# Kernel tuning notes

Hardware: AMD Instinct MI355X
Metric: run time of the kernel (lower is better)

The kernel has to match this reference:

```python
import jax, jax.numpy as jnp
import numpy as np

N, E, G = 50000, 1600000, 512
IN, HID, PROJ = 128, 128, 256


def setup_inputs() -> dict:
    key = jax.random.key(0)
    ks = jax.random.split(key, 20)
    s = 0.05
    return {
        'x1': jax.random.normal(ks[0], (N, IN), jnp.float32),
        'edge_index1': jax.random.randint(ks[1], (2, E), 0, N),
        'batch1': jnp.sort(jax.random.randint(ks[2], (N,), 0, G)),
        'x2': jax.random.normal(ks[3], (N, IN), jnp.float32),
        'edge_index2': jax.random.randint(ks[4], (2, E), 0, N),
        'batch2': jnp.sort(jax.random.randint(ks[5], (N,), 0, G)),
        'W1': jax.random.normal(ks[6], (IN, HID), jnp.float32) * s,
        'b1': jnp.zeros((HID,), jnp.float32),
        'W2': jax.random.normal(ks[7], (HID, HID), jnp.float32) * s,
        'b2': jnp.zeros((HID,), jnp.float32),
        'W3': jax.random.normal(ks[8], (HID, HID), jnp.float32) * s,
        'b3': jnp.zeros((HID,), jnp.float32),
        'Wp1': jax.random.normal(ks[9], (HID, PROJ), jnp.float32) * s,
        'bp1': jnp.zeros((PROJ,), jnp.float32),
        'gamma1': jnp.ones((PROJ,), jnp.float32),
        'beta1': jnp.zeros((PROJ,), jnp.float32),
        'Wp2': jax.random.normal(ks[10], (PROJ, PROJ), jnp.float32) * s,
        'bp2': jnp.zeros((PROJ,), jnp.float32),
        'gamma2': jnp.ones((PROJ,), jnp.float32),
        'beta2': jnp.zeros((PROJ,), jnp.float32),
        'Wq1': jax.random.normal(ks[11], (PROJ, PROJ // 2), jnp.float32) * s,
        'bq1': jnp.zeros((PROJ // 2,), jnp.float32),
        'Wq2': jax.random.normal(ks[12], (PROJ // 2, PROJ), jnp.float32) * s,
        'bq2': jnp.zeros((PROJ,), jnp.float32),
    }


def _gcn_conv(x, src, dst, W, b):
    # PyG GCNConv: add self-loops, symmetric norm, gather -> scatter-add
    n = x.shape[0]
    h = x @ W                                   # [n, out]
    loop = jnp.arange(n)
    s = jnp.concatenate([src, loop])
    d = jnp.concatenate([dst, loop])
    deg = jax.ops.segment_sum(jnp.ones(s.shape[0], h.dtype), d, num_segments=n)
    dinv = jnp.where(deg > 0, 1.0 / jnp.sqrt(deg), 0.0)
    norm = (dinv[s] * dinv[d])[:, None]         # [E+n, 1]
    out = jax.ops.segment_sum(h[s] * norm, d, num_segments=n)
    return out + b


def _encode(x, edge_index, batch, W1, b1, W2, b2, W3, b3):
    src, dst = edge_index[0], edge_index[1]
    h = jax.nn.relu(_gcn_conv(x, src, dst, W1, b1))
    h = jax.nn.relu(_gcn_conv(h, src, dst, W2, b2)) + h
    h = jax.nn.relu(_gcn_conv(h, src, dst, W3, b3)) + h
    # global mean pool over graph ids
    s = jax.ops.segment_sum(h, batch, num_segments=G)
    cnt = jax.ops.segment_sum(jnp.ones(h.shape[0], h.dtype), batch, num_segments=G)
    return s / jnp.maximum(cnt, 1.0)[:, None]


def _batchnorm(x, gamma, beta):
    m = x.mean(axis=0)
    v = x.var(axis=0)  # biased, matches torch BN normalization
    return gamma * (x - m) / jnp.sqrt(v + 1e-5) + beta


def _projector(h, Wp1, bp1, g1, be1, Wp2, bp2, g2, be2):
    z = jax.nn.relu(_batchnorm(h @ Wp1 + bp1, g1, be1))
    return _batchnorm(z @ Wp2 + bp2, g2, be2)


def _predictor(z, Wq1, bq1, Wq2, bq2):
    return jax.nn.relu(z @ Wq1 + bq1) @ Wq2 + bq2


def reference(x1, edge_index1, batch1, x2, edge_index2, batch2,
              W1, b1, W2, b2, W3, b3,
              Wp1, bp1, gamma1, beta1, Wp2, bp2, gamma2, beta2,
              Wq1, bq1, Wq2, bq2):
    h1 = _encode(x1, edge_index1, batch1, W1, b1, W2, b2, W3, b3)
    h2 = _encode(x2, edge_index2, batch2, W1, b1, W2, b2, W3, b3)
    z1 = _projector(h1, Wp1, bp1, gamma1, beta1, Wp2, bp2, gamma2, beta2)
    z2 = _projector(h2, Wp1, bp1, gamma1, beta1, Wp2, bp2, gamma2, beta2)
    p1 = _predictor(z1, Wq1, bq1, Wq2, bq2)
    p2 = _predictor(z2, Wq1, bq1, Wq2, bq2)
    return (p1, p2, z1, z2)
```

## Files before the change

kernel.cpp:

```cpp
#include <hip/hip_runtime.h>
#include <hip/hip_bf16.h>

#define NN     50000
#define NN2    100000
#define NEDGE  1600000
#define NE2    3200000
#define NG     512
#define FIN    128
#define FHID   128
#define FPROJ  256

#define BSH    9
#define BSZ    512
#define NBUCK  98
#define NBUCK2 196
#define EPB    8192
#define NABLK  196
#define NABLK2 392
#define NHIST2 (NBUCK2*NABLK2)
#define NSB1   ((NHIST2 + 255) / 256)

#define SRCSH  12
#define NKEY   (BSZ * 16)

#define MAXE_BLK 2048

typedef __attribute__((ext_vector_type(8))) short short8;
typedef __attribute__((ext_vector_type(4))) float f32x4;
typedef __attribute__((ext_vector_type(2))) float f32x2;

static __device__ __forceinline__ short f2bf(float f) {
    union { float f; unsigned u; } x; x.f = f;
    unsigned r = (x.u + 0x7FFFu + ((x.u >> 16) & 1u)) >> 16;
    return (short)(r & 0xFFFFu);
}
static __device__ __forceinline__ float bf2f(unsigned short u) {
    union { unsigned u; float f; } x; x.u = ((unsigned)u) << 16;
    return x.f;
}
static __device__ __forceinline__ float bflo(unsigned u) {
    union { unsigned u; float f; } x; x.u = u << 16; return x.f;
}
static __device__ __forceinline__ float bfhi(unsigned u) {
    union { unsigned u; float f; } x; x.u = u & 0xFFFF0000u; return x.f;
}
static __device__ __forceinline__ unsigned packbf(float a, float b) {
    return (unsigned)(unsigned short)f2bf(a) | ((unsigned)(unsigned short)f2bf(b) << 16);
}
static __device__ __forceinline__ f32x2 bfpair(unsigned u) {
    union { unsigned v[2]; f32x2 f; } x;
    x.v[0] = u << 16;
    x.v[1] = u & 0xFFFF0000u;
    return x.f;
}


__global__ __launch_bounds__(1024) void k_bhist(const int* __restrict__ dst0,
                                                const int* __restrict__ dst1,
                                                int* __restrict__ histG,
                                                unsigned short* __restrict__ lrank,
                                                const float* __restrict__ W0,
                                                const float* __restrict__ W1,
                                                const float* __restrict__ W2,
                                                short* __restrict__ Wf) {
    if (blockIdx.x >= NABLK2) {
        int w = (blockIdx.x - NABLK2) * 1024 + threadIdx.x;
        int l = w >> 11;
        int t = w & 2047;
        int b = t >> 6;
        int lane = t & 63;
        const float* W = (l == 0) ? W0 : (l == 1) ? W1 : W2;
        int nt = b >> 2, kt = b & 3;
        int n = nt * 16 + (lane & 15);
        int kbase = kt * 32 + (lane >> 4) * 8;
        short8 v;
#pragma unroll
        for (int j = 0; j < 8; ++j) v[j] = f2bf(W[(kbase + j) * FHID + n]);
        *(short8*)(Wf + (size_t)l * 16384 + (size_t)((nt * 4 + kt) * 64 + lane) * 8) = v;
        return;
    }
    __shared__ int h[NBUCK2];
    for (int j = threadIdx.x; j < NBUCK2; j += 1024) h[j] = 0;
    __syncthreads();
    int b = blockIdx.x;
    int g = b / NABLK, blk = b % NABLK;
    const int* dst = g ? dst1 : dst0;
    int base = blk * EPB;
    int gb = g * NBUCK;
    for (int t = threadIdx.x; t < EPB; t += 1024) {
        int i = base + t;
        if (i < NEDGE)
            lrank[(size_t)g * NEDGE + i] =
                (unsigned short)atomicAdd(&h[gb + (dst[i] >> BSH)], 1);
    }
    __syncthreads();
    for (int j = threadIdx.x; j < NBUCK2; j += 1024)
        histG[(size_t)j * NABLK2 + b] = h[j];
}

__global__ void s_scan256(const int* __restrict__ in, int* __restrict__ out,
                          int* __restrict__ bsum, int n) {
    __shared__ int s[256];
    int i = blockIdx.x * 256 + threadIdx.x;
    int v = (i < n) ? in[i] : 0;
    s[threadIdx.x] = v;
    for (int o = 1; o < 256; o <<= 1) {
        __syncthreads();
        int t = (threadIdx.x >= o) ? s[threadIdx.x - o] : 0;
        __syncthreads();
        s[threadIdx.x] += t;
    }
    __syncthreads();
    if (i < n) out[i] = s[threadIdx.x] - v;
    if (threadIdx.x == 255) bsum[blockIdx.x] = s[255];
}

__global__ __launch_bounds__(512) void s_scan_tail(int* __restrict__ bsum, int nb) {
    __shared__ int s[512];
    int v = (threadIdx.x < nb) ? bsum[threadIdx.x] : 0;
    s[threadIdx.x] = v;
    for (int o = 1; o < 512; o <<= 1) {
        __syncthreads();
        int t = (threadIdx.x >= o) ? s[threadIdx.x - o] : 0;
        __syncthreads();
        s[threadIdx.x] += t;
    }
    __syncthreads();
    if (threadIdx.x < nb) bsum[threadIdx.x] = s[threadIdx.x] - v;
}

__global__ void s_add(int* __restrict__ out, const int* __restrict__ bs, int n) {
    int i = blockIdx.x * 256 + threadIdx.x;
    if (i < n) out[i] += bs[blockIdx.x];
}

__global__ __launch_bounds__(1024) void k_part(const int* __restrict__ src0,
                                               const int* __restrict__ dst0,
                                               const int* __restrict__ src1,
                                               const int* __restrict__ dst1,
                                               const unsigned short* __restrict__ lrank,
                                               const int* __restrict__ histS,
                                               unsigned* __restrict__ pedge) {
    int b = blockIdx.x;
    int g = b / NABLK, blk = b % NABLK;
    const int* src = g ? src1 : src0;
    const int* dst = g ? dst1 : dst0;
    int base = blk * EPB;
    int gb = g * NBUCK;
    for (int t = threadIdx.x; t < EPB; t += 1024) {
        int i = base + t;
        if (i < NEDGE) {
            int d = dst[i];
            int pos = histS[(size_t)(gb + (d >> BSH)) * NABLK2 + b]
                      + (int)lrank[(size_t)g * NEDGE + i];
            pedge[pos] = (unsigned)src[i] | ((unsigned)(d & (BSZ - 1)) << 16);
        }
    }
}

__global__ __launch_bounds__(512) void k_csr(const unsigned* __restrict__ pedge,
                                             const int* __restrict__ histS,
                                             int* __restrict__ csroff,
                                             unsigned short* __restrict__ csrc,
                                             float* __restrict__ dinv) {
    __shared__ int cnt[NKEY];
    __shared__ int part[512];
    int k = blockIdx.x;
    int g = k / NBUCK;
    int nl0 = (k - g * NBUCK) * BSZ;
    int beg = histS[(size_t)k * NABLK2];
    int end = (k == NBUCK2 - 1) ? NE2 : histS[(size_t)(k + 1) * NABLK2];
    int t = threadIdx.x;
    for (int j = t; j < NKEY; j += 512) cnt[j] = 0;
    __syncthreads();
    for (int e = beg + t; e < end; e += 512) {
        unsigned v = pedge[e];
        int key = (int)((v >> 16) << 4) | (int)((v & 0xFFFFu) >> SRCSH);
        atomicAdd(&cnt[key], 1);
    }
    __syncthreads();
    int base = t * 16;
    int s = 0;
#pragma unroll
    for (int j = 0; j < 16; ++j) s += cnt[base + j];
    part[t] = s;
    for (int o = 1; o < 512; o <<= 1) {
        __syncthreads();
        int v2 = (t >= o) ? part[t - o] : 0;
        __syncthreads();
        part[t] += v2;
    }
    __syncthreads();
    int run = part[t] - s;
#pragma unroll
    for (int j = 0; j < 16; ++j) { int c = cnt[base + j]; cnt[base + j] = run; run += c; }
    __syncthreads();
    {
        int nl = nl0 + t;
        if (nl < NN) {
            int gn = g * NN + nl;
            int d0 = cnt[t * 16];
            int d1 = (t == BSZ - 1) ? (end - beg) : cnt[(t + 1) * 16];
            csroff[gn] = beg + d0;
            dinv[gn] = 1.0f / sqrtf((float)(d1 - d0 + 1));
        }
    }
    __syncthreads();
    for (int e = beg + t; e < end; e += 512) {
        unsigned v = pedge[e];
        int key = (int)((v >> 16) << 4) | (int)((v & 0xFFFFu) >> SRCSH);
        int r = atomicAdd(&cnt[key], 1);
        csrc[beg + r] = (unsigned short)(v & 0xFFFFu);
    }
    if (k == NBUCK2 - 1 && t == 0) csroff[NN2] = NE2;
}


__global__ __launch_bounds__(256) void k_gemm(const float* __restrict__ x1,
                                              const float* __restrict__ x2,
                                              const unsigned short* __restrict__ Abf,
                                              const short* __restrict__ Wf,
                                              const float* __restrict__ dinv,
                                              unsigned short* __restrict__ hp) {
    int lane = threadIdx.x & 63;
    int wv = threadIdx.x >> 6;
    int quad = lane >> 4;
    int rowbase = blockIdx.x * 64 + wv * 16;
    int arow = rowbase + (lane & 15);
    if (arow >= NN2) arow = NN2 - 1;

    f32x4 acc[8];
#pragma unroll
    for (int i = 0; i < 8; ++i) acc[i] = (f32x4){0.f, 0.f, 0.f, 0.f};

#pragma unroll
    for (int kt = 0; kt < 4; ++kt) {
        short8 af;
        if (Abf) {
            af = *(const short8*)(Abf + (size_t)arow * FIN + kt * 32 + quad * 8);
        } else {
            const float* ap = (arow < NN ? x1 + (size_t)arow * FIN
                                         : x2 + (size_t)(arow - NN) * FIN)
                              + kt * 32 + quad * 8;
            float4 a0 = *(const float4*)ap;
            float4 a1 = *(const float4*)(ap + 4);
            af[0] = f2bf(a0.x); af[1] = f2bf(a0.y); af[2] = f2bf(a0.z); af[3] = f2bf(a0.w);
            af[4] = f2bf(a1.x); af[5] = f2bf(a1.y); af[6] = f2bf(a1.z); af[7] = f2bf(a1.w);
        }
#pragma unroll
        for (int nt = 0; nt < 8; ++nt) {
            short8 bf = *(const short8*)(Wf + (size_t)((nt * 4 + kt) * 64 + lane) * 8);
            acc[nt] = __builtin_amdgcn_mfma_f32_16x16x32_bf16(af, bf, acc[nt], 0, 0, 0);
        }
    }
    float4 dv = *(const float4*)(dinv + rowbase + quad * 4);
    float dvv[4] = {dv.x, dv.y, dv.z, dv.w};
    int col = lane & 15;
#pragma unroll
    for (int r = 0; r < 4; ++r) {
        int orow = rowbase + quad * 4 + r;
        if (orow < NN2) {
#pragma unroll
            for (int nt = 0; nt < 8; ++nt)
                hp[(size_t)orow * FHID + nt * 16 + col] =
                    (unsigned short)f2bf(acc[nt][r] * dvv[r]);
        }
    }
}


#define RDI(S, EE) { _Pragma("unroll") for (int j = 0; j < 4; ++j) S[j] = (int)sidx[(EE) + j]; }
#define GTH(V, S)  { _Pragma("unroll") for (int j = 0; j < 4; ++j) V[j] = hpg[(size_t)S[j] * 16 + l16]; }
#define ACC4(V)    { _Pragma("unroll") for (int j = 0; j < 4; ++j) { \
                       a0 += bfpair(V[j].x); a1 += bfpair(V[j].y);   \
                       a2 += bfpair(V[j].z); a3 += bfpair(V[j].w); } }

__global__ __launch_bounds__(256) void k_agg(const uint4* __restrict__ hp4,
                                             const int* __restrict__ off,
                                             const unsigned short* __restrict__ csrc,
                                             const float* __restrict__ dinv,
                                             const float* __restrict__ bias,
                                             const unsigned short* __restrict__ resid,
                                             unsigned short* __restrict__ hout) {
    __shared__ unsigned short sidx[MAXE_BLK + 16];
    int tid = threadIdx.x;
    int l16 = tid & 15;
    int grp = tid >> 4;
    int gnb = blockIdx.x * 16;
    int blkBeg = off[gnb];
    int blkLen = off[gnb + 16] - blkBeg;
    if (blkLen > MAXE_BLK) blkLen = MAXE_BLK;
    for (int i = tid; i < blkLen; i += 256)
        sidx[i] = csrc[blkBeg + i];
    __syncthreads();

    int gn = gnb + grp;
    int g = gn >= NN;
    int node = gn - g * NN;
    const uint4* hpg = hp4 + (size_t)g * NN * 16;
    int beg = off[gn], end = off[gn + 1];
    int lbeg = beg - blkBeg;

    uint4 sv = hpg[(size_t)node * 16 + l16];
    f32x2 a0 = (f32x2){0.f, 0.f}, a1 = (f32x2){0.f, 0.f};
    f32x2 a2 = (f32x2){0.f, 0.f}, a3 = (f32x2){0.f, 0.f};

    int n4 = (end - beg) >> 2;
    if (n4 >= 2) {
        int s0[4], s1[4];
        uint4 v0[4], v1[4];
        int e = lbeg;
        RDI(s0, e);
        RDI(s1, e + 4);
        GTH(v0, s0);
        e += 8;
        int k = 1;
        while (k + 2 <= n4) {
            GTH(v1, s1);
            RDI(s0, e); e += 4;
            ACC4(v0);
            GTH(v0, s0);
            RDI(s1, e); e += 4;
            ACC4(v1);
            k += 2;
        }
        if (k < n4) {
            GTH(v1, s1);
            ACC4(v0);
            ACC4(v1);
        } else {
            ACC4(v0);
        }
    } else if (n4 == 1) {
        int s0[4]; uint4 v0[4];
        RDI(s0, lbeg);
        GTH(v0, s0);
        ACC4(v0);
    }
    int et = lbeg + (n4 << 2), lend = lbeg + (end - beg);
    for (; et < lend; ++et) {
        uint4 w = hpg[(size_t)sidx[et] * 16 + l16];
        a0 += bfpair(w.x); a1 += bfpair(w.y); a2 += bfpair(w.z); a3 += bfpair(w.w);
    }
    a0 += bfpair(sv.x); a1 += bfpair(sv.y); a2 += bfpair(sv.z); a3 += bfpair(sv.w);

    float dv = dinv[gn];
    float4 b0 = ((const float4*)bias)[l16 * 2];
    float4 b1 = ((const float4*)bias)[l16 * 2 + 1];
    float o0 = fmaxf(a0.x * dv + b0.x, 0.f);
    float o1 = fmaxf(a0.y * dv + b0.y, 0.f);
    float o2 = fmaxf(a1.x * dv + b0.z, 0.f);
    float o3 = fmaxf(a1.y * dv + b0.w, 0.f);
    float o4 = fmaxf(a2.x * dv + b1.x, 0.f);
    float o5 = fmaxf(a2.y * dv + b1.y, 0.f);
    float o6 = fmaxf(a3.x * dv + b1.z, 0.f);
    float o7 = fmaxf(a3.y * dv + b1.w, 0.f);
    if (resid) {
        uint4 rv = ((const uint4*)resid)[(size_t)gn * 16 + l16];
        o0 += bflo(rv.x); o1 += bfhi(rv.x);
        o2 += bflo(rv.y); o3 += bfhi(rv.y);
        o4 += bflo(rv.z); o5 += bfhi(rv.z);
        o6 += bflo(rv.w); o7 += bfhi(rv.w);
    }
    uint4 ov;
    ov.x = packbf(o0, o1);
    ov.y = packbf(o2, o3);
    ov.z = packbf(o4, o5);
    ov.w = packbf(o6, o7);
    ((uint4*)hout)[(size_t)gn * 16 + l16] = ov;
}


static __device__ __forceinline__ int lbound(const int* __restrict__ a, int key) {
    int lo = 0, hi = NN;
    while (lo < hi) { int mid = (lo + hi) >> 1; if (a[mid] < key) lo = mid + 1; else hi = mid; }
    return lo;
}

__global__ void k_pool(const unsigned short* __restrict__ h,
                       const int* __restrict__ b0, const int* __restrict__ b1,
                       float* __restrict__ pooled, float* __restrict__ stats) {
    int b = blockIdx.x;
    int g = b >> 9, lg = b & 511;
    int c = threadIdx.x;
    if (b == 0) {
        for (int i = c; i < 2048; i += 128) stats[i] = 0.f;
    }
    const int* batch = g ? b1 : b0;
    int beg = lbound(batch, lg);
    int end = lbound(batch, lg + 1);
    const unsigned short* hb = h + (size_t)g * NN * FHID;
    float s = 0.f;
    for (int i = beg; i < end; ++i) s += bf2f(hb[(size_t)i * FHID + c]);
    int cnt = end - beg;
    pooled[(size_t)b * FHID + c] = s / (float)(cnt > 0 ? cnt : 1);
}


template<int NC>
__global__ __launch_bounds__(256) void k_head(const float* __restrict__ A,
                                              const float* __restrict__ W,
                                              const float* __restrict__ bias,
                                              float* __restrict__ out,
                                              int K, int act,
                                              float* __restrict__ statsOut,
                                              const float* __restrict__ statsIn,
                                              const float* __restrict__ gIn,
                                              const float* __restrict__ beIn,
                                              int bnRelu, float* __restrict__ zout) {
    constexpr int NGRP = 256 / NC;
    constexpr int RPG  = 4 / NGRP;
    __shared__ float As[4 * 256];
    __shared__ float scl[256], shf[256];
    int t = threadIdx.x;
    int c = t & (NC - 1);
    int rg = t / NC;
    int r0 = blockIdx.x * 4;
    int g = (r0 >= NG) ? 1 : 0;
    if (statsIn) {
        const float* si = statsIn + g * 512;
        for (int j = t; j < K; j += 256) {
            float m = si[j] * (1.f / 512.f);
            float var = si[K + j] * (1.f / 512.f) - m * m;
            float inv = 1.0f / sqrtf(var + 1e-5f);
            float s = gIn[j] * inv;
            scl[j] = s;
            shf[j] = beIn[j] - m * s;
        }
    }
    __syncthreads();
    for (int idx = t; idx < 4 * K; idx += 256) {
        float v = A[(size_t)r0 * K + idx];
        if (statsIn) {
            int k = idx & (K - 1);
            v = v * scl[k] + shf[k];
            if (bnRelu) v = fmaxf(v, 0.f);
        }
        if (zout) zout[(size_t)r0 * K + idx] = v;
        As[idx] = v;
    }
    __syncthreads();
    float bb = bias[c];
    float acc[RPG];
#pragma unroll
    for (int r = 0; r < RPG; ++r) acc[r] = bb;
    const float* Ab = As + (rg * RPG) * K;
    for (int k = 0; k < K; k += 8) {
        float w0 = W[(size_t)(k + 0) * NC + c];
        float w1 = W[(size_t)(k + 1) * NC + c];
        float w2 = W[(size_t)(k + 2) * NC + c];
        float w3 = W[(size_t)(k + 3) * NC + c];
        float w4 = W[(size_t)(k + 4) * NC + c];
        float w5 = W[(size_t)(k + 5) * NC + c];
        float w6 = W[(size_t)(k + 6) * NC + c];
        float w7 = W[(size_t)(k + 7) * NC + c];
#pragma unroll
        for (int r = 0; r < RPG; ++r) {
            float4 a0 = *(const float4*)(Ab + r * K + k);
            float4 a1 = *(const float4*)(Ab + r * K + k + 4);
            acc[r] = fmaf(a0.x, w0, acc[r]);
            acc[r] = fmaf(a0.y, w1, acc[r]);
            acc[r] = fmaf(a0.z, w2, acc[r]);
            acc[r] = fmaf(a0.w, w3, acc[r]);
            acc[r] = fmaf(a1.x, w4, acc[r]);
            acc[r] = fmaf(a1.y, w5, acc[r]);
            acc[r] = fmaf(a1.z, w6, acc[r]);
            acc[r] = fmaf(a1.w, w7, acc[r]);
        }
    }
    if (statsOut) {
        float s = 0.f, q = 0.f;
#pragma unroll
        for (int r = 0; r < RPG; ++r) { s += acc[r]; q += acc[r] * acc[r]; }
        atomicAdd(&statsOut[g * 512 + c], s);
        atomicAdd(&statsOut[g * 512 + NC + c], q);
    }
#pragma unroll
    for (int r = 0; r < RPG; ++r) {
        float v = acc[r];
        if (act) v = fmaxf(v, 0.f);
        out[(size_t)(r0 + rg * RPG + r) * NC + c] = v;
    }
}


extern "C" void kernel_launch(void* const* d_in, const int* in_sizes, int n_in,
                              void* d_out, int out_size, void* d_ws, size_t ws_size,
                              hipStream_t stream) {
    const float* x1 = (const float*)d_in[0];
    const float* x2 = (const float*)d_in[3];
    const int*   ei[2]    = {(const int*)d_in[1], (const int*)d_in[4]};
    const int*   batch[2] = {(const int*)d_in[2], (const int*)d_in[5]};
    const float* W[3]  = {(const float*)d_in[6], (const float*)d_in[8], (const float*)d_in[10]};
    const float* bb[3] = {(const float*)d_in[7], (const float*)d_in[9], (const float*)d_in[11]};
    const float* Wp1 = (const float*)d_in[12]; const float* bp1 = (const float*)d_in[13];
    const float* g1  = (const float*)d_in[14]; const float* be1 = (const float*)d_in[15];
    const float* Wp2 = (const float*)d_in[16]; const float* bp2 = (const float*)d_in[17];
    const float* g2  = (const float*)d_in[18]; const float* be2 = (const float*)d_in[19];
    const float* Wq1 = (const float*)d_in[20]; const float* bq1 = (const float*)d_in[21];
    const float* Wq2 = (const float*)d_in[22]; const float* bq2 = (const float*)d_in[23];

    char* ws = (char*)d_ws;
    size_t off = 0;
    auto alloc = [&](size_t bytes) -> void* {
        void* p = ws + off;
        off += (bytes + 255) & ~(size_t)255;
        return p;
    };
    unsigned short* h_cur  = (unsigned short*)alloc((size_t)NN2 * FHID * 2);
    unsigned short* hp     = (unsigned short*)alloc((size_t)NN2 * FHID * 2);
    unsigned short* csrc   = (unsigned short*)alloc((size_t)(NE2 + 16) * 2);
    int*            csroff = (int*)alloc((size_t)(NN2 + 1) * 4);
    unsigned short* lrank  = (unsigned short*)alloc((size_t)NE2 * 2);
    unsigned*       pedge  = (unsigned*)alloc((size_t)NE2 * 4);
    int*            histG  = (int*)alloc((size_t)NHIST2 * 4);
    int*            histS  = (int*)alloc((size_t)NHIST2 * 4);
    int*            bsum   = (int*)alloc(512 * 4);
    float*          dinv   = (float*)alloc((size_t)100352 * 4);
    float*          pooled = (float*)alloc((size_t)2 * NG * FHID * 4);
    short*          Wf     = (short*)alloc((size_t)3 * 16384 * 2);
    float*          t1     = (float*)alloc((size_t)1024 * 256 * 4);
    float*          t2     = (float*)alloc((size_t)1024 * 256 * 4);
    float*          t3     = (float*)alloc((size_t)1024 * 128 * 4);
    float*          stats  = (float*)alloc(2048 * 4);

    const int* src0 = ei[0];           const int* dst0 = ei[0] + NEDGE;
    const int* src1 = ei[1];           const int* dst1 = ei[1] + NEDGE;

    k_bhist<<<NABLK2 + 6, 1024, 0, stream>>>(dst0, dst1, histG, lrank,
                                             W[0], W[1], W[2], Wf);
    s_scan256<<<NSB1, 256, 0, stream>>>(histG, histS, bsum, NHIST2);
    s_scan_tail<<<1, 512, 0, stream>>>(bsum, NSB1);
    s_add<<<NSB1, 256, 0, stream>>>(histS, bsum, NHIST2);
    k_part<<<NABLK2, 1024, 0, stream>>>(src0, dst0, src1, dst1, lrank, histS, pedge);
    k_csr<<<NBUCK2, 512, 0, stream>>>(pedge, histS, csroff, csrc, dinv);

    for (int l = 0; l < 3; ++l) {
        const unsigned short* Abf = (l == 0) ? nullptr : h_cur;
        const unsigned short* resid = (l == 0) ? nullptr : h_cur;
        k_gemm<<<1564, 256, 0, stream>>>(x1, x2, Abf, Wf + (size_t)l * 16384, dinv, hp);
        k_agg<<<6250, 256, 0, stream>>>((const uint4*)hp, csroff, csrc, dinv,
                                        bb[l], resid, h_cur);
    }
    k_pool<<<1024, 128, 0, stream>>>(h_cur, batch[0], batch[1], pooled, stats);

    float* outp = (float*)d_out;
    float* p_out = outp;
    float* z_out = outp + (size_t)2 * NG * FPROJ;
    float* st1 = stats, *st2 = stats + 1024;
    k_head<256><<<256, 256, 0, stream>>>(pooled, Wp1, bp1, t1, 128, 0,
                                         st1, nullptr, nullptr, nullptr, 0, nullptr);
    k_head<256><<<256, 256, 0, stream>>>(t1, Wp2, bp2, t2, 256, 0,
                                         st2, st1, g1, be1, 1, nullptr);
    k_head<128><<<256, 256, 0, stream>>>(t2, Wq1, bq1, t3, 256, 1,
                                         nullptr, st2, g2, be2, 0, z_out);
    k_head<256><<<256, 256, 0, stream>>>(t3, Wq2, bq2, p_out, 128, 0,
                                         nullptr, nullptr, nullptr, nullptr, 0, nullptr);
}
```

Baseline: 635.8 us.

## Fuse pooling into first head GEMM, fold scan add into consumers, pin gather schedule

Removes the s_add kernel by having k_part and k_csr add the block-sum offset when they read histS. It also fuses mean pooling into the first projector GEMM as k_head_pool, which drops the pooled buffer and one launch, and moves stats zeroing into k_bhist. Sched barriers are added after the gathers in k_agg so the loads are issued ahead of the accumulates. In exchange the pooling runs with fewer threads per graph, and the stats layout must match the g*512 indexing the later kernels expect.

```diff
diff --git a/kernel.cpp b/kernel.cpp
--- a/kernel.cpp
+++ b/kernel.cpp
@@ -62,8 +62,13 @@
                                                 const float* __restrict__ W0,
                                                 const float* __restrict__ W1,
                                                 const float* __restrict__ W2,
-                                                short* __restrict__ Wf) {
+                                                short* __restrict__ Wf,
+                                                float* __restrict__ stats) {
     if (blockIdx.x >= NABLK2) {
+        if (blockIdx.x == NABLK2) {
+            stats[threadIdx.x] = 0.f;
+            stats[threadIdx.x + 1024] = 0.f;
+        }
         int w = (blockIdx.x - NABLK2) * 1024 + threadIdx.x;
         int l = w >> 11;
         int t = w & 2047;
@@ -129,17 +134,13 @@
     if (threadIdx.x < nb) bsum[threadIdx.x] = s[threadIdx.x] - v;
 }
 
-__global__ void s_add(int* __restrict__ out, const int* __restrict__ bs, int n) {
-    int i = blockIdx.x * 256 + threadIdx.x;
-    if (i < n) out[i] += bs[blockIdx.x];
-}
-
 __global__ __launch_bounds__(1024) void k_part(const int* __restrict__ src0,
                                                const int* __restrict__ dst0,
                                                const int* __restrict__ src1,
                                                const int* __restrict__ dst1,
                                                const unsigned short* __restrict__ lrank,
                                                const int* __restrict__ histS,
+                                               const int* __restrict__ bsum,
                                                unsigned* __restrict__ pedge) {
     int b = blockIdx.x;
     int g = b / NABLK, blk = b % NABLK;
@@ -151,7 +152,8 @@
         int i = base + t;
         if (i < NEDGE) {
             int d = dst[i];
-            int pos = histS[(size_t)(gb + (d >> BSH)) * NABLK2 + b]
+            int idx = (gb + (d >> BSH)) * NABLK2 + b;
+            int pos = histS[idx] + bsum[idx >> 8]
                       + (int)lrank[(size_t)g * NEDGE + i];
             pedge[pos] = (unsigned)src[i] | ((unsigned)(d & (BSZ - 1)) << 16);
         }
@@ -160,6 +162,7 @@
 
 __global__ __launch_bounds__(512) void k_csr(const unsigned* __restrict__ pedge,
                                              const int* __restrict__ histS,
+                                             const int* __restrict__ bsumG,
                                              int* __restrict__ csroff,
                                              unsigned short* __restrict__ csrc,
                                              float* __restrict__ dinv) {
@@ -168,8 +171,11 @@
     int k = blockIdx.x;
     int g = k / NBUCK;
     int nl0 = (k - g * NBUCK) * BSZ;
-    int beg = histS[(size_t)k * NABLK2];
-    int end = (k == NBUCK2 - 1) ? NE2 : histS[(size_t)(k + 1) * NABLK2];
+    int i0 = k * NABLK2;
+    int beg = histS[i0] + bsumG[i0 >> 8];
+    int end;
+    if (k == NBUCK2 - 1) end = NE2;
+    else { int i1 = (k + 1) * NABLK2; end = histS[i1] + bsumG[i1 >> 8]; }
     int t = threadIdx.x;
     for (int j = t; j < NKEY; j += 512) cnt[j] = 0;
     __syncthreads();
@@ -269,6 +275,7 @@
 }
 
 
+#define SCHB __builtin_amdgcn_sched_barrier(0)
 #define RDI(S, EE) { _Pragma("unroll") for (int j = 0; j < 4; ++j) S[j] = (int)sidx[(EE) + j]; }
 #define GTH(V, S)  { _Pragma("unroll") for (int j = 0; j < 4; ++j) V[j] = hpg[(size_t)S[j] * 16 + l16]; }
 #define ACC4(V)    { _Pragma("unroll") for (int j = 0; j < 4; ++j) { \
@@ -312,20 +319,20 @@
         int e = lbeg;
         RDI(s0, e);
         RDI(s1, e + 4);
-        GTH(v0, s0);
+        GTH(v0, s0); SCHB;
         e += 8;
         int k = 1;
         while (k + 2 <= n4) {
-            GTH(v1, s1);
+            GTH(v1, s1); SCHB;
             RDI(s0, e); e += 4;
             ACC4(v0);
-            GTH(v0, s0);
+            GTH(v0, s0); SCHB;
             RDI(s1, e); e += 4;
             ACC4(v1);
             k += 2;
         }
         if (k < n4) {
-            GTH(v1, s1);
+            GTH(v1, s1); SCHB;
             ACC4(v0);
             ACC4(v1);
         } else {
@@ -377,23 +384,70 @@
     return lo;
 }
 
-__global__ void k_pool(const unsigned short* __restrict__ h,
-                       const int* __restrict__ b0, const int* __restrict__ b1,
-                       float* __restrict__ pooled, float* __restrict__ stats) {
-    int b = blockIdx.x;
-    int g = b >> 9, lg = b & 511;
-    int c = threadIdx.x;
-    if (b == 0) {
-        for (int i = c; i < 2048; i += 128) stats[i] = 0.f;
-    }
+__global__ __launch_bounds__(256) void k_head_pool(const unsigned short* __restrict__ h,
+                                                   const int* __restrict__ b0,
+                                                   const int* __restrict__ b1,
+                                                   const float* __restrict__ W,
+                                                   const float* __restrict__ bias,
+                                                   float* __restrict__ out,
+                                                   float* __restrict__ statsOut) {
+    __shared__ float As[4 * 128];
+    __shared__ int bnds[5];
+    int t = threadIdx.x;
+    int r0 = blockIdx.x * 4;
+    int g = (r0 >= NG) ? 1 : 0;
+    int lg0 = r0 & (NG - 1);
     const int* batch = g ? b1 : b0;
-    int beg = lbound(batch, lg);
-    int end = lbound(batch, lg + 1);
-    const unsigned short* hb = h + (size_t)g * NN * FHID;
-    float s = 0.f;
-    for (int i = beg; i < end; ++i) s += bf2f(hb[(size_t)i * FHID + c]);
-    int cnt = end - beg;
-    pooled[(size_t)b * FHID + c] = s / (float)(cnt > 0 ? cnt : 1);
+    if (t < 5) bnds[t] = lbound(batch, lg0 + t);
+    __syncthreads();
+    {
+        int c = t & 127, half = t >> 7;
+        const unsigned short* hb = h + (size_t)g * NN * FHID;
+        for (int rr = 0; rr < 2; ++rr) {
+            int r = half * 2 + rr;
+            int beg = bnds[r], end = bnds[r + 1];
+            float s = 0.f;
+            for (int i = beg; i < end; ++i) s += bf2f(hb[(size_t)i * FHID + c]);
+            int cnt = end - beg;
+            As[r * 128 + c] = s / (float)(cnt > 0 ? cnt : 1);
+        }
+    }
+    __syncthreads();
+    float bb = bias[t];
+    float acc[4] = {bb, bb, bb, bb};
+    for (int k = 0; k < 128; k += 8) {
+        float w0 = W[(size_t)(k + 0) * 256 + t];
+        float w1 = W[(size_t)(k + 1) * 256 + t];
+        float w2 = W[(size_t)(k + 2) * 256 + t];
+        float w3 = W[(size_t)(k + 3) * 256 + t];
+        float w4 = W[(size_t)(k + 4) * 256 + t];
+        float w5 = W[(size_t)(k + 5) * 256 + t];
+        float w6 = W[(size_t)(k + 6) * 256 + t];
+        float w7 = W[(size_t)(k + 7) * 256 + t];
+#pragma unroll
+        for (int r = 0; r < 4; ++r) {
+            float4 q0 = *(const float4*)(As + r * 128 + k);
+            float4 q1 = *(const float4*)(As + r * 128 + k + 4);
+            acc[r] = fmaf(q0.x, w0, acc[r]);
+            acc[r] = fmaf(q0.y, w1, acc[r]);
+            acc[r] = fmaf(q0.z, w2, acc[r]);
+            acc[r] = fmaf(q0.w, w3, acc[r]);
+            acc[r] = fmaf(q1.x, w4, acc[r]);
+            acc[r] = fmaf(q1.y, w5, acc[r]);
+            acc[r] = fmaf(q1.z, w6, acc[r]);
+            acc[r] = fmaf(q1.w, w7, acc[r]);
+        }
+    }
+    {
+        float s = 0.f, q = 0.f;
+#pragma unroll
+        for (int r = 0; r < 4; ++r) { s += acc[r]; q += acc[r] * acc[r]; }
+        atomicAdd(&statsOut[g * 512 + t], s);
+        atomicAdd(&statsOut[g * 512 + 256 + t], q);
+    }
+#pragma unroll
+    for (int r = 0; r < 4; ++r)
+        out[(size_t)(r0 + r) * 256 + t] = acc[r];
 }
 
 
@@ -517,7 +571,6 @@
     int*            histS  = (int*)alloc((size_t)NHIST2 * 4);
     int*            bsum   = (int*)alloc(512 * 4);
     float*          dinv   = (float*)alloc((size_t)100352 * 4);
-    float*          pooled = (float*)alloc((size_t)2 * NG * FHID * 4);
     short*          Wf     = (short*)alloc((size_t)3 * 16384 * 2);
     float*          t1     = (float*)alloc((size_t)1024 * 256 * 4);
     float*          t2     = (float*)alloc((size_t)1024 * 256 * 4);
@@ -528,12 +581,12 @@
     const int* src1 = ei[1];           const int* dst1 = ei[1] + NEDGE;
 
     k_bhist<<<NABLK2 + 6, 1024, 0, stream>>>(dst0, dst1, histG, lrank,
-                                             W[0], W[1], W[2], Wf);
+                                             W[0], W[1], W[2], Wf, stats);
     s_scan256<<<NSB1, 256, 0, stream>>>(histG, histS, bsum, NHIST2);
     s_scan_tail<<<1, 512, 0, stream>>>(bsum, NSB1);
-    s_add<<<NSB1, 256, 0, stream>>>(histS, bsum, NHIST2);
-    k_part<<<NABLK2, 1024, 0, stream>>>(src0, dst0, src1, dst1, lrank, histS, pedge);
-    k_csr<<<NBUCK2, 512, 0, stream>>>(pedge, histS, csroff, csrc, dinv);
+    k_part<<<NABLK2, 1024, 0, stream>>>(src0, dst0, src1, dst1, lrank, histS,
+                                        bsum, pedge);
+    k_csr<<<NBUCK2, 512, 0, stream>>>(pedge, histS, bsum, csroff, csrc, dinv);
 
     for (int l = 0; l < 3; ++l) {
         const unsigned short* Abf = (l == 0) ? nullptr : h_cur;
@@ -542,14 +595,13 @@
         k_agg<<<6250, 256, 0, stream>>>((const uint4*)hp, csroff, csrc, dinv,
                                         bb[l], resid, h_cur);
     }
-    k_pool<<<1024, 128, 0, stream>>>(h_cur, batch[0], batch[1], pooled, stats);
 
     float* outp = (float*)d_out;
     float* p_out = outp;
     float* z_out = outp + (size_t)2 * NG * FPROJ;
     float* st1 = stats, *st2 = stats + 1024;
-    k_head<256><<<256, 256, 0, stream>>>(pooled, Wp1, bp1, t1, 128, 0,
-                                         st1, nullptr, nullptr, nullptr, 0, nullptr);
+    k_head_pool<<<256, 256, 0, stream>>>(h_cur, batch[0], batch[1],
+                                         Wp1, bp1, t1, st1);
     k_head<256><<<256, 256, 0, stream>>>(t1, Wp2, bp2, t2, 256, 0,
                                          st2, st1, g1, be1, 1, nullptr);
     k_head<128><<<256, 256, 0, stream>>>(t2, Wq1, bq1, t3, 256, 1,
```

After: 658.2 us. +3.5%, slower.
